# Performance work log

Hardware: AMD Instinct MI355X
Metric: run time of the kernel (lower is better)

The kernel has to match this reference:

```python
import jax, jax.numpy as jnp
import numpy as np

B, S, D, E = 32, 16, 64, 768  # batch, max summary segments, max doc splits, embed dim
EPS = 1e-12


def _l2norm(x):
    # tf.nn.l2_normalize: x * rsqrt(max(sum(x^2), eps))
    return x * jax.lax.rsqrt(jnp.maximum(jnp.sum(x * x, axis=-1, keepdims=True), EPS))


def setup_inputs() -> dict:
    key = jax.random.key(0)
    ks = jax.random.split(key, 12)
    nd = jax.random.randint(ks[0], (B,), 1, D + 1)
    ns = jax.random.randint(ks[1], (B,), 1, S + 1)
    doc = jax.random.normal(ks[2], (B, D, E), jnp.float32)
    seg = jax.random.normal(ks[3], (B, S, E), jnp.float32)
    # emulate RaggedTensor.to_tensor(): zero padding beyond ragged lengths
    doc = doc * (jnp.arange(D)[None, :, None] < nd[:, None, None])
    seg = seg * (jnp.arange(S)[None, :, None] < ns[:, None, None])
    tis = jax.random.uniform(ks[4], (B, S), jnp.float32)
    tis = jnp.where(jnp.arange(S)[None, :] < ns[:, None], tis, 1.0)
    tagg = jax.random.uniform(ks[5], (B,), jnp.float32)
    s1, s2, s3 = 1.0 / np.sqrt(2 * E), 1.0 / np.sqrt(E), 1.0 / np.sqrt(E // 2)
    W1 = jax.random.normal(ks[6], (2 * E, E), jnp.float32) * s1
    W2 = jax.random.normal(ks[7], (E, E // 2), jnp.float32) * s2
    W3 = jax.random.normal(ks[8], (E // 2, 1), jnp.float32) * s3
    return {
        'document_splits_embedding': doc,
        'summary_sentences_embedding': seg,
        'num_document_splits': nd,
        'num_summary_segments': ns,
        'target_agg_score': tagg,
        'target_instance_score': tis,
        'W1': W1, 'b1': jnp.zeros((E,), jnp.float32),
        'W2': W2, 'b2': jnp.zeros((E // 2,), jnp.float32),
        'W3': W3, 'b3': jnp.zeros((1,), jnp.float32),
    }


def reference(document_splits_embedding, summary_sentences_embedding,
              num_document_splits, num_summary_segments,
              target_agg_score, target_instance_score,
              W1, b1, W2, b2, W3, b3):
    doc, seg = document_splits_embedding, summary_sentences_embedding
    nd, ns = num_document_splits, num_summary_segments
    b, d, e = doc.shape
    s = seg.shape[1]
    nsf = ns.astype(jnp.float32)

    # target_instance_score padded with 1.0 beyond ragged length (done in setup; pass through)
    tis = target_instance_score

    # ---- pairwise MLP over all (segment, doc_split) pairs ----
    pair = jnp.concatenate([
        jnp.broadcast_to(doc[:, None, :, :], (b, s, d, e)),
        jnp.broadcast_to(seg[:, :, None, :], (b, s, d, e)),
    ], axis=-1)                                             # [B,S,D,2E]
    h = jax.nn.gelu(pair @ W1 + b1, approximate=False)      # [B,S,D,E]
    h = jax.nn.gelu(h @ W2 + b2, approximate=False)         # [B,S,D,E/2]
    mlp_out = jax.nn.sigmoid(h @ W3 + b3)[..., 0]           # [B,S,D]

    doc_mask = (jnp.arange(d)[None, :] < nd[:, None]).astype(jnp.float32)  # [B,D]
    scored = doc_mask[:, None, :] * mlp_out                # mask invalid doc splits
    pred0 = jnp.max(scored, axis=2)                         # [B,S]
    seg_scale = jnp.where(ns > 10, 1.0, 100.0)[:, None]     # faithful to mask+(1-mask)*100
    pred = seg_scale * pred0                                # [B,S]

    # ---- cosine similarity prior (keras CosineSimilarity = -cos) ----
    dn = _l2norm(doc)                                       # [B,D,E]
    sn = _l2norm(seg)                                       # [B,S,E]
    cos = jnp.einsum('bse,bde->bsd', sn, dn)                # [B,S,D]
    sim = doc_mask[:, None, :] * (1.0 + (-cos)) / 2.0
    doc_cos = jnp.max(sim, axis=2)                          # [B,S]
    seg_mask = (jnp.arange(s)[None, :] < ns[:, None]).astype(jnp.float32)
    diff = jnp.abs(doc_cos - pred) * seg_mask
    cos_prior = jnp.mean(jnp.sum(diff, axis=1) / nsf)

    # ---- correlation prior: Pearson correlation over the 768 'sample' axis ----
    c = seg - jnp.mean(seg, axis=-1, keepdims=True)
    z = c * jax.lax.rsqrt(jnp.maximum(jnp.sum(c * c, axis=-1, keepdims=True), EPS))
    R = (1.0 + jnp.einsum('bse,bte->bst', z, z)) / 2.0      # [B,S,S]
    p = pred
    t1 = (1.0 - p)[:, :, None] * (1.0 - p)[:, None, :]
    t2 = p[:, :, None] * p[:, None, :]
    pair_mask = seg_mask[:, :, None] * seg_mask[:, None, :]
    term = jnp.abs(t1 - R) * jnp.abs(t2 - R) * pair_mask
    corr_prior = jnp.mean(jnp.sum(term, axis=(1, 2)) / nsf)

    return (target_agg_score, tis, pred, ns, cos_prior, corr_prior)
```

## Files before the change

kernel.cpp:

```cpp
#include <hip/hip_runtime.h>
#include <hip/hip_bf16.h>
#include <math.h>

#define EPSF 1e-12f

typedef short bf16x8 __attribute__((ext_vector_type(8)));
typedef float f32x4  __attribute__((ext_vector_type(4)));

__device__ __forceinline__ float gelu_fast(float x) {
    float x2 = x * x;
    float z = -2.3021184f * x * fmaf(0.044715f, x2, 1.0f);
    float u = __builtin_amdgcn_exp2f(z);
    return x * __builtin_amdgcn_rcpf(1.0f + u);
}
__device__ __forceinline__ float sigmoid_fast(float x) {
    float u = __builtin_amdgcn_exp2f(-1.44269504f * x);
    return __builtin_amdgcn_rcpf(1.0f + u);
}
__device__ __forceinline__ float bf2f(unsigned short u) {
    return __uint_as_float(((unsigned int)u) << 16);
}
__device__ __forceinline__ unsigned short f2bf(float f) {
    unsigned int u = __float_as_uint(f);
    u += 0x7FFFu + ((u >> 16) & 1u);
    return (unsigned short)(u >> 16);
}

__global__ __launch_bounds__(256) void k_prep(
    const float* __restrict__ doc, const float* __restrict__ seg,
    const float* __restrict__ W1, const float* __restrict__ W2,
    const float* __restrict__ tagg, const float* __restrict__ tis,
    const int* __restrict__ ns,
    float* __restrict__ dscale, float* __restrict__ sscale,
    float* __restrict__ smean, float* __restrict__ cscale,
    unsigned short* __restrict__ docB, unsigned short* __restrict__ segB,
    unsigned short* __restrict__ W1T, unsigned short* __restrict__ W2T,
    float* __restrict__ out)
{
    __shared__ float sT[64][65];
    int blk = blockIdx.x;
    int t = threadIdx.x;
    if (blk == 1000) {
        if (t < 32) out[t] = tagg[t];
        out[32 + t] = tis[t];
        out[32 + 256 + t] = tis[256 + t];
        if (t < 32) out[1056 + t] = (float)ns[t];
        return;
    }
    if (blk < 640) {
        int row = blk * 4 + (t >> 6);
        int lane = t & 63;
        const float* src = (row < 2048) ? (doc + (size_t)row * 768)
                                        : (seg + (size_t)(row - 2048) * 768);
        unsigned short* dst = (row < 2048) ? (docB + (size_t)row * 768)
                                           : (segB + (size_t)(row - 2048) * 768);
        float ss = 0.f, sm = 0.f;
        float xv[12];
        #pragma unroll
        for (int i = 0; i < 12; ++i) {
            float x = src[lane + 64 * i];
            xv[i] = x;
            ss += x * x; sm += x;
        }
        #pragma unroll
        for (int i = 0; i < 12; ++i) dst[lane + 64 * i] = f2bf(xv[i]);
        #pragma unroll
        for (int off = 32; off > 0; off >>= 1) {
            ss += __shfl_down(ss, off);
            sm += __shfl_down(sm, off);
        }
        if (lane == 0) {
            if (row < 2048) {
                dscale[row] = rsqrtf(fmaxf(ss, EPSF));
            } else {
                int r = row - 2048;
                sscale[r] = rsqrtf(fmaxf(ss, EPSF));
                float mean = sm * (1.0f / 768.0f);
                smean[r] = mean;
                cscale[r] = rsqrtf(fmaxf(ss - sm * mean, EPSF));
            }
        }
        return;
    }
    int tt = blk - 640;
    const float* in; unsigned short* out2; int R, C, bx, by;
    if (tt < 288) { in = W1; out2 = W1T; R = 1536; C = 768; bx = tt % 12; by = tt / 12; }
    else { tt -= 288; in = W2; out2 = W2T; R = 768; C = 384; bx = tt % 6; by = tt / 6; }
    int c0 = bx * 64, r0 = by * 64;
    int tr = t >> 2, tc4 = (t & 3) * 16;
    #pragma unroll
    for (int i = 0; i < 4; ++i) {
        float4 v = *(const float4*)(in + (size_t)(r0 + tr) * C + c0 + tc4 + i * 4);
        sT[tr][tc4 + i * 4 + 0] = v.x; sT[tr][tc4 + i * 4 + 1] = v.y;
        sT[tr][tc4 + i * 4 + 2] = v.z; sT[tr][tc4 + i * 4 + 3] = v.w;
    }
    __syncthreads();
    union { uint4 v; unsigned short u[8]; } o0, o1;
    #pragma unroll
    for (int i = 0; i < 8; ++i) o0.u[i] = f2bf(sT[tc4 + i][tr]);
    #pragma unroll
    for (int i = 0; i < 8; ++i) o1.u[i] = f2bf(sT[tc4 + 8 + i][tr]);
    *(uint4*)(out2 + (size_t)(c0 + tr) * R + r0 + tc4) = o0.v;
    *(uint4*)(out2 + (size_t)(c0 + tr) * R + r0 + tc4 + 8) = o1.v;
}

__global__ __launch_bounds__(256) void k_l1(
    const unsigned short* __restrict__ docB, const unsigned short* __restrict__ segB,
    const unsigned short* __restrict__ W1T_bf, const float* __restrict__ b1,
    unsigned short* __restrict__ XdocB, unsigned short* __restrict__ XsegB)
{
    int mb = blockIdx.x;
    int n0 = blockIdx.y * 128;
    int t = threadIdx.x, w = t >> 6, l = t & 63;
    int lm = l & 15, kh = l >> 4;
    bool isdoc = (mb < 32);
    int m0 = isdoc ? mb * 64 : (mb - 32) * 64;
    const unsigned short* A = isdoc ? docB : segB;
    int koff = isdoc ? 0 : 768;
    unsigned short* C = isdoc ? XdocB : XsegB;

    const unsigned short* gA = A + (size_t)(m0 + lm) * 768 + kh * 8;
    const unsigned short* gB = W1T_bf + (size_t)(n0 + w * 32 + lm) * 1536 + koff + kh * 8;

    f32x4 acc[4][2];
    #pragma unroll
    for (int mt = 0; mt < 4; ++mt)
        #pragma unroll
        for (int nt = 0; nt < 2; ++nt) acc[mt][nt] = (f32x4){0.f, 0.f, 0.f, 0.f};

    bf16x8 aA[4], aB[4], bA[2], bB[2];
    #pragma unroll
    for (int mt = 0; mt < 4; ++mt) aA[mt] = *(const bf16x8*)(gA + (size_t)mt * 16 * 768);
    #pragma unroll
    for (int nt = 0; nt < 2; ++nt) bA[nt] = *(const bf16x8*)(gB + (size_t)nt * 16 * 1536);

    for (int kt = 0; kt < 12; ++kt) {
        int ko1 = kt * 64 + 32;
        #pragma unroll
        for (int mt = 0; mt < 4; ++mt) aB[mt] = *(const bf16x8*)(gA + (size_t)mt * 16 * 768 + ko1);
        #pragma unroll
        for (int nt = 0; nt < 2; ++nt) bB[nt] = *(const bf16x8*)(gB + (size_t)nt * 16 * 1536 + ko1);
        #pragma unroll
        for (int mt = 0; mt < 4; ++mt)
            #pragma unroll
            for (int nt = 0; nt < 2; ++nt)
                acc[mt][nt] = __builtin_amdgcn_mfma_f32_16x16x32_bf16(
                    aA[mt], bA[nt], acc[mt][nt], 0, 0, 0);
        if (kt < 11) {
            int ko2 = kt * 64 + 64;
            #pragma unroll
            for (int mt = 0; mt < 4; ++mt) aA[mt] = *(const bf16x8*)(gA + (size_t)mt * 16 * 768 + ko2);
            #pragma unroll
            for (int nt = 0; nt < 2; ++nt) bA[nt] = *(const bf16x8*)(gB + (size_t)nt * 16 * 1536 + ko2);
        }
        #pragma unroll
        for (int mt = 0; mt < 4; ++mt)
            #pragma unroll
            for (int nt = 0; nt < 2; ++nt)
                acc[mt][nt] = __builtin_amdgcn_mfma_f32_16x16x32_bf16(
                    aB[mt], bB[nt], acc[mt][nt], 0, 0, 0);
    }
    #pragma unroll
    for (int nt = 0; nt < 2; ++nt) {
        int n = n0 + w * 32 + nt * 16 + lm;
        float bv = isdoc ? 0.f : b1[n];
        #pragma unroll
        for (int mt = 0; mt < 4; ++mt)
            #pragma unroll
            for (int j = 0; j < 4; ++j) {
                int row = m0 + mt * 16 + kh * 4 + j;
                C[(size_t)row * 768 + n] = f2bf(acc[mt][nt][j] + bv);
            }
    }
}

__global__ __launch_bounds__(256, 2) void k_fused_mfma(
    const unsigned short* __restrict__ XdocB, const unsigned short* __restrict__ XsegB,
    const unsigned short* __restrict__ W2T_bf,
    const float* __restrict__ b2, const float* __restrict__ W3, const float* __restrict__ b3,
    const int* __restrict__ nd, const int* __restrict__ ns,
    const unsigned short* __restrict__ docB, const unsigned short* __restrict__ segB,
    const float* __restrict__ seg,
    const float* __restrict__ dscale, const float* __restrict__ sscale,
    const float* __restrict__ smean, const float* __restrict__ cscale,
    float* __restrict__ out_pred, float* __restrict__ predv,
    float* __restrict__ dcws, float* __restrict__ Rws)
{
    __shared__ union {
        struct {
            unsigned short sA0[64 * 64];
            unsigned short sA1[64 * 64];
            float sXseg[768];
            float sRed[64][4];
        } p;
        struct { float sRedC[16][4]; } c;
        struct { unsigned short zb[16][776]; } r;
    } U;

    int blk = blockIdx.x;
    int t = threadIdx.x, w = t >> 6, l = t & 63;
    int lm = l & 15, kh = l >> 4;

    if (blk >= 512) {
        if (blk < 544) {
            int b = blk - 512;
            const unsigned short* gS = segB + (size_t)(b * 16 + lm) * 768 + kh * 8;
            const unsigned short* gD = docB + (size_t)(b * 64 + w * 16 + lm) * 768 + kh * 8;
            f32x4 acc = (f32x4){0.f, 0.f, 0.f, 0.f};
            for (int kt = 0; kt < 24; ++kt) {
                bf16x8 a = *(const bf16x8*)(gS + kt * 32);
                bf16x8 bb = *(const bf16x8*)(gD + kt * 32);
                acc = __builtin_amdgcn_mfma_f32_16x16x32_bf16(a, bb, acc, 0, 0, 0);
            }
            int ndb = nd[b];
            int d = w * 16 + lm;
            float dsc = dscale[b * 64 + d];
            #pragma unroll
            for (int j = 0; j < 4; ++j) {
                int s = kh * 4 + j;
                float cosv = acc[j] * sscale[b * 16 + s] * dsc;
                float sim = (d < ndb) ? (1.0f - cosv) * 0.5f : 0.f;
                sim = fmaxf(sim, __shfl_xor(sim, 1));
                sim = fmaxf(sim, __shfl_xor(sim, 2));
                sim = fmaxf(sim, __shfl_xor(sim, 4));
                sim = fmaxf(sim, __shfl_xor(sim, 8));
                if (lm == 0) U.c.sRedC[s][w] = sim;
            }
            __syncthreads();
            if (t < 16) {
                float dc = fmaxf(fmaxf(U.c.sRedC[t][0], U.c.sRedC[t][1]),
                                 fmaxf(U.c.sRedC[t][2], U.c.sRedC[t][3]));
                dcws[b * 16 + t] = dc;
            }
        } else {
            int b = blk - 544;
            for (int i = t; i < 16 * 768; i += 256) {
                int s = i / 768; int e = i - s * 768;
                U.r.zb[s][e] = f2bf((seg[((size_t)b * 16 + s) * 768 + e]
                                     - smean[b * 16 + s]) * cscale[b * 16 + s]);
            }
            __syncthreads();
            if (w == 0) {
                f32x4 acc = (f32x4){0.f, 0.f, 0.f, 0.f};
                #pragma unroll
                for (int kt = 0; kt < 24; ++kt) {
                    bf16x8 z = *(const bf16x8*)&U.r.zb[lm][kt * 32 + kh * 8];
                    acc = __builtin_amdgcn_mfma_f32_16x16x32_bf16(z, z, acc, 0, 0, 0);
                }
                #pragma unroll
                for (int j = 0; j < 4; ++j) {
                    int row = kh * 4 + j;
                    Rws[b * 256 + row * 16 + lm] = 0.5f * (1.0f + acc[j]);
                }
            }
        }
        return;
    }

    int bs = blk;
    int b = bs >> 4;
    int sw2 = (lm & 7) << 4;

    for (int i = t; i < 768; i += 256) U.p.sXseg[i] = bf2f(XsegB[(size_t)bs * 768 + i]);

    const int ndb = nd[b];
    const float segscale = (ns[b] > 10) ? 1.0f : 100.0f;
    const float b3v = b3[0];

    f32x4 acc[4][6];
    #pragma unroll
    for (int mt = 0; mt < 4; ++mt)
        #pragma unroll
        for (int nt = 0; nt < 6; ++nt) acc[mt][nt] = (f32x4){0.f, 0.f, 0.f, 0.f};

    int ar = t >> 2, ak = (t & 3) * 16;
    int asw = (ar & 7) << 4;
    const char* gXd = (const char*)XdocB + (size_t)(b * 64 + ar) * 1536;
    const unsigned short* gW2w = W2T_bf + (size_t)(w * 96 + lm) * 768 + kh * 8;

    union u128 { uint4 v; unsigned short u[8]; };

    bf16x8 bbA[6], bbB[6];
    #pragma unroll
    for (int nt = 0; nt < 6; ++nt)
        bbA[nt] = *(const bf16x8*)(gW2w + (size_t)nt * 16 * 768);

    {
        u128 xc0, xc1;
        xc0.v = *(const uint4*)(gXd + ak * 2);
        xc1.v = *(const uint4*)(gXd + ak * 2 + 16);
        __syncthreads();
        u128 o0, o1;
        #pragma unroll
        for (int i = 0; i < 8; ++i)
            o0.u[i] = f2bf(gelu_fast(bf2f(xc0.u[i]) + U.p.sXseg[ak + i]));
        #pragma unroll
        for (int i = 0; i < 8; ++i)
            o1.u[i] = f2bf(gelu_fast(bf2f(xc1.u[i]) + U.p.sXseg[ak + 8 + i]));
        *(uint4*)((char*)U.p.sA0 + ar * 128 + ((ak * 2) ^ asw)) = o0.v;
        *(uint4*)((char*)U.p.sA0 + ar * 128 + ((ak * 2 + 16) ^ asw)) = o1.v;
    }

    #pragma unroll
    for (int kt = 0; kt < 12; ++kt) {
        unsigned short* cbuf = (kt & 1) ? U.p.sA1 : U.p.sA0;
        unsigned short* nbuf = (kt & 1) ? U.p.sA0 : U.p.sA1;
        __syncthreads();
        u128 xn0, xn1;
        if (kt < 11) {
            xn0.v = *(const uint4*)(gXd + (kt + 1) * 128 + ak * 2);
            xn1.v = *(const uint4*)(gXd + (kt + 1) * 128 + ak * 2 + 16);
        }
        {
            #pragma unroll
            for (int nt = 0; nt < 6; ++nt)
                bbB[nt] = *(const bf16x8*)(gW2w + (size_t)nt * 16 * 768 + kt * 64 + 32);
            int kb = (kh * 16) ^ sw2;
            bf16x8 a[4];
            #pragma unroll
            for (int mt = 0; mt < 4; ++mt)
                a[mt] = *(const bf16x8*)((const char*)cbuf + (mt * 16 + lm) * 128 + kb);
            #pragma unroll
            for (int mt = 0; mt < 4; ++mt)
                #pragma unroll
                for (int nt = 0; nt < 6; ++nt)
                    acc[mt][nt] = __builtin_amdgcn_mfma_f32_16x16x32_bf16(
                        a[mt], bbA[nt], acc[mt][nt], 0, 0, 0);
        }
        {
            if (kt < 11) {
                #pragma unroll
                for (int nt = 0; nt < 6; ++nt)
                    bbA[nt] = *(const bf16x8*)(gW2w + (size_t)nt * 16 * 768 + (kt + 1) * 64);
            }
            int kb = (64 + kh * 16) ^ sw2;
            bf16x8 a[4];
            #pragma unroll
            for (int mt = 0; mt < 4; ++mt)
                a[mt] = *(const bf16x8*)((const char*)cbuf + (mt * 16 + lm) * 128 + kb);
            #pragma unroll
            for (int mt = 0; mt < 4; ++mt)
                #pragma unroll
                for (int nt = 0; nt < 6; ++nt)
                    acc[mt][nt] = __builtin_amdgcn_mfma_f32_16x16x32_bf16(
                        a[mt], bbB[nt], acc[mt][nt], 0, 0, 0);
        }
        if (kt < 11) {
            u128 o0, o1;
            #pragma unroll
            for (int i = 0; i < 8; ++i)
                o0.u[i] = f2bf(gelu_fast(bf2f(xn0.u[i]) + U.p.sXseg[(kt + 1) * 64 + ak + i]));
            #pragma unroll
            for (int i = 0; i < 8; ++i)
                o1.u[i] = f2bf(gelu_fast(bf2f(xn1.u[i]) + U.p.sXseg[(kt + 1) * 64 + ak + 8 + i]));
            *(uint4*)((char*)nbuf + ar * 128 + ((ak * 2) ^ asw)) = o0.v;
            *(uint4*)((char*)nbuf + ar * 128 + ((ak * 2 + 16) ^ asw)) = o1.v;
        }
    }

    float b2v[6], w3v[6];
    #pragma unroll
    for (int nt = 0; nt < 6; ++nt) {
        int n = w * 96 + nt * 16 + lm;
        b2v[nt] = b2[n]; w3v[nt] = W3[n];
    }
    #pragma unroll
    for (int mt = 0; mt < 4; ++mt) {
        #pragma unroll
        for (int j = 0; j < 4; ++j) {
            float s = 0.f;
            #pragma unroll
            for (int nt = 0; nt < 6; ++nt)
                s += gelu_fast(acc[mt][nt][j] + b2v[nt]) * w3v[nt];
            s += __shfl_xor(s, 1); s += __shfl_xor(s, 2);
            s += __shfl_xor(s, 4); s += __shfl_xor(s, 8);
            if (lm == 0) U.p.sRed[mt * 16 + kh * 4 + j][w] = s;
        }
    }
    __syncthreads();
    if (w == 0) {
        float h3 = U.p.sRed[l][0] + U.p.sRed[l][1] + U.p.sRed[l][2] + U.p.sRed[l][3] + b3v;
        float sig = sigmoid_fast(h3);
        float val = (l < ndb) ? sig : 0.f;
        #pragma unroll
        for (int off = 32; off > 0; off >>= 1) val = fmaxf(val, __shfl_xor(val, off));
        if (l == 0) {
            float pv = segscale * val;
            out_pred[bs] = pv;
            predv[bs] = pv;
        }
    }
}

__global__ __launch_bounds__(256) void k_final(
    const int* __restrict__ ns, const float* __restrict__ dcws,
    const float* __restrict__ Rws, const float* __restrict__ predv,
    float* __restrict__ out)
{
    __shared__ float sl1[32], sl2[32];
    int t = threadIdx.x;
    if (t < 32) {
        int nsb = ns[t];
        float sb = 0.f;
        #pragma unroll
        for (int s = 0; s < 16; ++s) {
            float d = fabsf(dcws[t * 16 + s] - predv[t * 16 + s]);
            sb += (s < nsb) ? d : 0.f;
        }
        sl1[t] = sb / (float)nsb;
    }
    {
        int b = t >> 3, c = t & 7;
        int nsb = ns[b];
        float sum = 0.f;
        #pragma unroll
        for (int k = 0; k < 32; ++k) {
            int idx = c * 32 + k;
            int s = idx >> 4, tt = idx & 15;
            float R = Rws[b * 256 + idx];
            float ps = predv[b * 16 + s], pt = predv[b * 16 + tt];
            float t1 = (1.f - ps) * (1.f - pt), t2 = ps * pt;
            float term = fabsf(t1 - R) * fabsf(t2 - R);
            sum += (s < nsb && tt < nsb) ? term : 0.f;
        }
        sum += __shfl_xor(sum, 1);
        sum += __shfl_xor(sum, 2);
        sum += __shfl_xor(sum, 4);
        if (c == 0) sl2[b] = sum / (float)nsb;
    }
    __syncthreads();
    if (t == 0) {
        float a = 0.f, bsum = 0.f;
        #pragma unroll
        for (int i = 0; i < 32; ++i) { a += sl1[i]; bsum += sl2[i]; }
        out[1088] = a * (1.0f / 32.0f);
        out[1089] = bsum * (1.0f / 32.0f);
    }
}

extern "C" void kernel_launch(void* const* d_in, const int* in_sizes, int n_in,
                              void* d_out, int out_size, void* d_ws, size_t ws_size,
                              hipStream_t stream)
{
    const float* doc  = (const float*)d_in[0];
    const float* seg  = (const float*)d_in[1];
    const int*   nd   = (const int*)d_in[2];
    const int*   ns   = (const int*)d_in[3];
    const float* tagg = (const float*)d_in[4];
    const float* tis  = (const float*)d_in[5];
    const float* W1   = (const float*)d_in[6];
    const float* b1   = (const float*)d_in[7];
    const float* W2   = (const float*)d_in[8];
    const float* b2   = (const float*)d_in[9];
    const float* W3   = (const float*)d_in[10];
    const float* b3   = (const float*)d_in[11];
    float* out = (float*)d_out;

    float* fws      = (float*)d_ws;
    float* dscale   = fws;
    float* sscale   = dscale + 2048;
    float* smean    = sscale + 512;
    float* cscale   = smean + 512;
    float* predv    = cscale + 512;
    float* dcws     = predv + 512;
    float* Rws      = dcws + 512;
    unsigned short* docB  = (unsigned short*)(Rws + 8192);
    unsigned short* segB  = docB + (size_t)2048 * 768;
    unsigned short* W1T   = segB + (size_t)512 * 768;
    unsigned short* W2T   = W1T + (size_t)768 * 1536;
    unsigned short* XdocB = W2T + (size_t)384 * 768;
    unsigned short* XsegB = XdocB + (size_t)2048 * 768;

    k_prep<<<1001, 256, 0, stream>>>(doc, seg, W1, W2, tagg, tis, ns,
                                     dscale, sscale, smean, cscale,
                                     docB, segB, W1T, W2T, out);
    k_l1<<<dim3(40, 6), 256, 0, stream>>>(docB, segB, W1T, b1, XdocB, XsegB);
    k_fused_mfma<<<576, 256, 0, stream>>>(XdocB, XsegB, W2T, b2, W3, b3, nd, ns,
                                          docB, segB, seg, dscale, sscale,
                                          smean, cscale, out + 544, predv,
                                          dcws, Rws);
    k_final<<<1, 256, 0, stream>>>(ns, dcws, Rws, predv, out);
}
```

Baseline: 83.98 us.

## Vectorize prep loads, deepen layer-1 GEMM prefetch, raise MFMA wave priority

```diff
diff --git a/kernel.cpp b/kernel.cpp
--- a/kernel.cpp
+++ b/kernel.cpp
@@ -55,15 +55,24 @@
         unsigned short* dst = (row < 2048) ? (docB + (size_t)row * 768)
                                            : (segB + (size_t)(row - 2048) * 768);
         float ss = 0.f, sm = 0.f;
-        float xv[12];
-        #pragma unroll
-        for (int i = 0; i < 12; ++i) {
-            float x = src[lane + 64 * i];
-            xv[i] = x;
-            ss += x * x; sm += x;
-        }
-        #pragma unroll
-        for (int i = 0; i < 12; ++i) dst[lane + 64 * i] = f2bf(xv[i]);
+        float4 v0 = *(const float4*)(src + lane * 4);
+        float4 v1 = *(const float4*)(src + lane * 4 + 256);
+        float4 v2 = *(const float4*)(src + lane * 4 + 512);
+        ss += v0.x * v0.x + v0.y * v0.y + v0.z * v0.z + v0.w * v0.w;
+        ss += v1.x * v1.x + v1.y * v1.y + v1.z * v1.z + v1.w * v1.w;
+        ss += v2.x * v2.x + v2.y * v2.y + v2.z * v2.z + v2.w * v2.w;
+        sm += v0.x + v0.y + v0.z + v0.w;
+        sm += v1.x + v1.y + v1.z + v1.w;
+        sm += v2.x + v2.y + v2.z + v2.w;
+        {
+            ushort4 o;
+            o.x = f2bf(v0.x); o.y = f2bf(v0.y); o.z = f2bf(v0.z); o.w = f2bf(v0.w);
+            *(ushort4*)(dst + lane * 4) = o;
+            o.x = f2bf(v1.x); o.y = f2bf(v1.y); o.z = f2bf(v1.z); o.w = f2bf(v1.w);
+            *(ushort4*)(dst + lane * 4 + 256) = o;
+            o.x = f2bf(v2.x); o.y = f2bf(v2.y); o.z = f2bf(v2.z); o.w = f2bf(v2.w);
+            *(ushort4*)(dst + lane * 4 + 512) = o;
+        }
         #pragma unroll
         for (int off = 32; off > 0; off >>= 1) {
             ss += __shfl_down(ss, off);
@@ -128,38 +137,54 @@
         #pragma unroll
         for (int nt = 0; nt < 2; ++nt) acc[mt][nt] = (f32x4){0.f, 0.f, 0.f, 0.f};
 
-    bf16x8 aA[4], aB[4], bA[2], bB[2];
-    #pragma unroll
-    for (int mt = 0; mt < 4; ++mt) aA[mt] = *(const bf16x8*)(gA + (size_t)mt * 16 * 768);
-    #pragma unroll
-    for (int nt = 0; nt < 2; ++nt) bA[nt] = *(const bf16x8*)(gB + (size_t)nt * 16 * 1536);
-
-    for (int kt = 0; kt < 12; ++kt) {
-        int ko1 = kt * 64 + 32;
-        #pragma unroll
-        for (int mt = 0; mt < 4; ++mt) aB[mt] = *(const bf16x8*)(gA + (size_t)mt * 16 * 768 + ko1);
-        #pragma unroll
-        for (int nt = 0; nt < 2; ++nt) bB[nt] = *(const bf16x8*)(gB + (size_t)nt * 16 * 1536 + ko1);
-        #pragma unroll
-        for (int mt = 0; mt < 4; ++mt)
-            #pragma unroll
-            for (int nt = 0; nt < 2; ++nt)
-                acc[mt][nt] = __builtin_amdgcn_mfma_f32_16x16x32_bf16(
-                    aA[mt], bA[nt], acc[mt][nt], 0, 0, 0);
-        if (kt < 11) {
-            int ko2 = kt * 64 + 64;
-            #pragma unroll
-            for (int mt = 0; mt < 4; ++mt) aA[mt] = *(const bf16x8*)(gA + (size_t)mt * 16 * 768 + ko2);
-            #pragma unroll
-            for (int nt = 0; nt < 2; ++nt) bA[nt] = *(const bf16x8*)(gB + (size_t)nt * 16 * 1536 + ko2);
-        }
-        #pragma unroll
-        for (int mt = 0; mt < 4; ++mt)
-            #pragma unroll
-            for (int nt = 0; nt < 2; ++nt)
-                acc[mt][nt] = __builtin_amdgcn_mfma_f32_16x16x32_bf16(
-                    aB[mt], bB[nt], acc[mt][nt], 0, 0, 0);
-    }
+    bf16x8 a0A[4], a1A[4], b0A[2], b1A[2];
+    bf16x8 a0B[4], a1B[4], b0B[2], b1B[2];
+    #pragma unroll
+    for (int mt = 0; mt < 4; ++mt) {
+        a0A[mt] = *(const bf16x8*)(gA + (size_t)mt * 16 * 768);
+        a1A[mt] = *(const bf16x8*)(gA + (size_t)mt * 16 * 768 + 32);
+    }
+    #pragma unroll
+    for (int nt = 0; nt < 2; ++nt) {
+        b0A[nt] = *(const bf16x8*)(gB + (size_t)nt * 16 * 1536);
+        b1A[nt] = *(const bf16x8*)(gB + (size_t)nt * 16 * 1536 + 32);
+    }
+
+    #define L1_BODY(KT, A0, A1, B0, B1, NA0, NA1, NB0, NB1)                     \
+    {                                                                           \
+        if ((KT) < 11) {                                                        \
+            int ko = ((KT) + 1) * 64;                                           \
+            _Pragma("unroll")                                                   \
+            for (int mt = 0; mt < 4; ++mt) {                                    \
+                NA0[mt] = *(const bf16x8*)(gA + (size_t)mt * 16 * 768 + ko);    \
+                NA1[mt] = *(const bf16x8*)(gA + (size_t)mt * 16 * 768 + ko + 32); \
+            }                                                                   \
+            _Pragma("unroll")                                                   \
+            for (int nt = 0; nt < 2; ++nt) {                                    \
+                NB0[nt] = *(const bf16x8*)(gB + (size_t)nt * 16 * 1536 + ko);   \
+                NB1[nt] = *(const bf16x8*)(gB + (size_t)nt * 16 * 1536 + ko + 32); \
+            }                                                                   \
+        }                                                                       \
+        _Pragma("unroll")                                                       \
+        for (int mt = 0; mt < 4; ++mt)                                          \
+            _Pragma("unroll")                                                   \
+            for (int nt = 0; nt < 2; ++nt)                                      \
+                acc[mt][nt] = __builtin_amdgcn_mfma_f32_16x16x32_bf16(          \
+                    A0[mt], B0[nt], acc[mt][nt], 0, 0, 0);                      \
+        _Pragma("unroll")                                                       \
+        for (int mt = 0; mt < 4; ++mt)                                          \
+            _Pragma("unroll")                                                   \
+            for (int nt = 0; nt < 2; ++nt)                                      \
+                acc[mt][nt] = __builtin_amdgcn_mfma_f32_16x16x32_bf16(          \
+                    A1[mt], B1[nt], acc[mt][nt], 0, 0, 0);                      \
+    }
+
+    for (int kt2 = 0; kt2 < 12; kt2 += 2) {
+        L1_BODY(kt2,     a0A, a1A, b0A, b1A, a0B, a1B, b0B, b1B);
+        L1_BODY(kt2 + 1, a0B, a1B, b0B, b1B, a0A, a1A, b0A, b1A);
+    }
+    #undef L1_BODY
+
     #pragma unroll
     for (int nt = 0; nt < 2; ++nt) {
         int n = n0 + w * 32 + nt * 16 + lm;
@@ -320,12 +345,14 @@
             #pragma unroll
             for (int mt = 0; mt < 4; ++mt)
                 a[mt] = *(const bf16x8*)((const char*)cbuf + (mt * 16 + lm) * 128 + kb);
+            __builtin_amdgcn_s_setprio(1);
             #pragma unroll
             for (int mt = 0; mt < 4; ++mt)
                 #pragma unroll
                 for (int nt = 0; nt < 6; ++nt)
                     acc[mt][nt] = __builtin_amdgcn_mfma_f32_16x16x32_bf16(
                         a[mt], bbA[nt], acc[mt][nt], 0, 0, 0);
+            __builtin_amdgcn_s_setprio(0);
         }
         {
             if (kt < 11) {
@@ -338,12 +365,14 @@
             #pragma unroll
             for (int mt = 0; mt < 4; ++mt)
                 a[mt] = *(const bf16x8*)((const char*)cbuf + (mt * 16 + lm) * 128 + kb);
+            __builtin_amdgcn_s_setprio(1);
             #pragma unroll
             for (int mt = 0; mt < 4; ++mt)
                 #pragma unroll
                 for (int nt = 0; nt < 6; ++nt)
                     acc[mt][nt] = __builtin_amdgcn_mfma_f32_16x16x32_bf16(
                         a[mt], bbB[nt], acc[mt][nt], 0, 0, 0);
+            __builtin_amdgcn_s_setprio(0);
         }
         if (kt < 11) {
             u128 o0, o1;
```

New measurement: 82.58 us, median of 2. About the same (-1.7%).
